# Kernel optimization log

Measured on AMD Instinct MI355X. Metric: run time of the kernel, lower is better.

The kernel has to match this reference:

```python
import jax, jax.numpy as jnp
import numpy as np

N, E, F0, H, D, G, C = 10000, 150000, 128, 8, 64, 64, 10
HD = H * D
SLOPE = 0.01  # LeakyReLU negative slope (alpha)
EPS = 1e-5    # BatchNorm eps


def gat_layer(x, src, dst, W, a_src, a_dst, b):
    # x: [N, Fin] -> out: [N, H*D]; standard multi-head GAT with concat
    n = x.shape[0]
    h = (x @ W).reshape(n, H, D)                       # [N,H,D]
    e_src = jnp.einsum('nhd,hd->nh', h, a_src)         # [N,H]
    e_dst = jnp.einsum('nhd,hd->nh', h, a_dst)
    e = e_src[src] + e_dst[dst]                        # [E,H]
    e = jnp.where(e > 0, e, SLOPE * e)                 # LeakyReLU
    m = jax.ops.segment_max(e, dst, num_segments=n)    # per-dst max for stable softmax
    ex = jnp.exp(e - m[dst])
    denom = jax.ops.segment_sum(ex, dst, num_segments=n)
    att = ex / denom[dst]                              # [E,H]
    msg = h[src] * att[:, :, None]                     # [E,H,D]
    out = jax.ops.segment_sum(msg, dst, num_segments=n).reshape(n, HD)
    return jax.nn.elu(out + b)


def hgnn_forward(x, edge_index, batch,
                 W0, as0, ad0, b0, W1, as1, ad1, b1,
                 W2, as2, ad2, b2, W3, as3, ad3, b3,
                 mW1, mb1, gamma, beta, mW2, mb2):
    src, dst = edge_index[0], edge_index[1]
    x0 = gat_layer(x, src, dst, W0, as0, ad0, b0)      # init_graph
    x1 = gat_layer(x0, src, dst, W1, as1, ad1, b1)     # head
    x2 = gat_layer(x1, src, dst, W2, as2, ad2, b2)     # body
    x3 = x0 + x2                                       # residual
    xt = gat_layer(x3, src, dst, W3, as3, ad3, b3)     # tail
    xc = jnp.concatenate((xt, x1, x2, x3), axis=1)     # [N, 4*HD]
    pooled = jax.ops.segment_max(xc, batch, num_segments=G)
    pooled = jnp.where(jnp.isfinite(pooled), pooled, 0.0)
    # MLP: Linear -> BatchNorm1d (batch-stats) -> ReLU -> Linear
    z = pooled @ mW1 + mb1
    mu = jnp.mean(z, axis=0)
    var = jnp.mean((z - mu) ** 2, axis=0)
    z = (z - mu) / jnp.sqrt(var + EPS) * gamma + beta
    z = jax.nn.relu(z)
    return z @ mW2 + mb2                               # [G, C]


def setup_inputs() -> dict:
    key = jax.random.key(0)
    ks = jax.random.split(key, 12)
    x = jax.random.normal(ks[0], (N, F0), jnp.float32)
    edge_index = jax.random.randint(ks[1], (2, E), 0, N, dtype=jnp.int32)
    batch = jnp.sort(jax.random.randint(ks[2], (N,), 0, G, dtype=jnp.int32))

    def layer_params(k, fin):
        k1, k2, k3 = jax.random.split(k, 3)
        return (0.1 * jax.random.normal(k1, (fin, HD), jnp.float32),
                0.1 * jax.random.normal(k2, (H, D), jnp.float32),
                0.1 * jax.random.normal(k3, (H, D), jnp.float32),
                jnp.zeros((HD,), jnp.float32))

    W0, as0, ad0, b0 = layer_params(ks[3], F0)
    W1, as1, ad1, b1 = layer_params(ks[4], HD)
    W2, as2, ad2, b2 = layer_params(ks[5], HD)
    W3, as3, ad3, b3 = layer_params(ks[6], HD)
    mW1 = 0.05 * jax.random.normal(ks[7], (4 * HD, HD), jnp.float32)
    mb1 = jnp.zeros((HD,), jnp.float32)
    gamma = jnp.ones((HD,), jnp.float32)
    beta = jnp.zeros((HD,), jnp.float32)
    mW2 = 0.05 * jax.random.normal(ks[8], (HD, C), jnp.float32)
    mb2 = jnp.zeros((C,), jnp.float32)
    return dict(x=x, edge_index=edge_index, batch=batch,
                W0=W0, as0=as0, ad0=ad0, b0=b0,
                W1=W1, as1=as1, ad1=ad1, b1=b1,
                W2=W2, as2=as2, ad2=ad2, b2=b2,
                W3=W3, as3=as3, ad3=ad3, b3=b3,
                mW1=mW1, mb1=mb1, gamma=gamma, beta=beta, mW2=mW2, mb2=mb2)


def reference(x, edge_index, batch,
              W0, as0, ad0, b0, W1, as1, ad1, b1,
              W2, as2, ad2, b2, W3, as3, ad3, b3,
              mW1, mb1, gamma, beta, mW2, mb2):
    return hgnn_forward(x, edge_index, batch,
                        W0, as0, ad0, b0, W1, as1, ad1, b1,
                        W2, as2, ad2, b2, W3, as3, ad3, b3,
                        mW1, mb1, gamma, beta, mW2, mb2)
```

## Files before the change

### kernel.cpp

```cpp
#include <hip/hip_runtime.h>

typedef unsigned short u16;
typedef __bf16 bfv8 __attribute__((ext_vector_type(8)));
typedef float f32x16 __attribute__((ext_vector_type(16)));

#define HDIM 512
#define NHEAD 8
#define GNUM 64
#define CNUM 10
#define SLOPE 0.01f
#define BNEPS 1e-5f
#define PSPLIT 8

__device__ __forceinline__ float b2f(u16 u) { return __uint_as_float(((unsigned)u) << 16); }
__device__ __forceinline__ u16 f2b(float f) {
    unsigned u = __float_as_uint(f);
    u += 0x7FFFu + ((u >> 16) & 1u);
    return (u16)(u >> 16);
}
__device__ __forceinline__ void splitbf(float v, u16& hi, u16& lo) {
    u16 h = f2b(v);
    hi = h;
    lo = f2b(v - b2f(h));
}

__global__ void sentinel_kernel(float* out, int n, float val) {
    int i = blockIdx.x * 256 + threadIdx.x;
    if (i < n) out[i] = val;
}

__global__ void zero_i32_kernel(int* __restrict__ p, int n) {
    int i = blockIdx.x * 256 + threadIdx.x;
    if (i < n) p[i] = 0;
}

__device__ __forceinline__ void wsplit_body(const float* __restrict__ W, u16* __restrict__ Whi,
                                            u16* __restrict__ Wlo, int K) {
    __shared__ float tile[64][65];
    int kb = blockIdx.x * 64, nb = blockIdx.y * 64;
    int t = threadIdx.x;
    #pragma unroll
    for (int i = 0; i < 16; i++) {
        int idx = t + i * 256;
        int r = idx >> 6, c = idx & 63;
        tile[r][c] = W[(size_t)(kb + r) * HDIM + nb + c];
    }
    __syncthreads();
    #pragma unroll
    for (int i = 0; i < 16; i++) {
        int idx = t + i * 256;
        int r = idx >> 6, c = idx & 63;
        float v = tile[c][r];
        u16 hi, lo;
        splitbf(v, hi, lo);
        size_t o = (size_t)(nb + r) * K + kb + c;
        Whi[o] = hi;
        Wlo[o] = lo;
    }
}

__global__ void wsplit_kernel(const float* __restrict__ W, u16* __restrict__ Whi,
                              u16* __restrict__ Wlo, int K) {
    wsplit_body(W, Whi, Wlo, K);
}

__global__ void wsplit3_kernel(const float* __restrict__ W1, const float* __restrict__ W2,
                               const float* __restrict__ W3,
                               u16* __restrict__ h1, u16* __restrict__ l1,
                               u16* __restrict__ h2, u16* __restrict__ l2,
                               u16* __restrict__ h3, u16* __restrict__ l3) {
    const float* W = (blockIdx.z == 0) ? W1 : (blockIdx.z == 1) ? W2 : W3;
    u16* Wh = (blockIdx.z == 0) ? h1 : (blockIdx.z == 1) ? h2 : h3;
    u16* Wl = (blockIdx.z == 0) ? l1 : (blockIdx.z == 1) ? l2 : l3;
    wsplit_body(W, Wh, Wl, HDIM);
}

__global__ void xsplit_kernel(const float* __restrict__ x, u16* __restrict__ hi,
                              u16* __restrict__ lo, int n) {
    int i = blockIdx.x * 256 + threadIdx.x;
    if (i < n) splitbf(x[i], hi[i], lo[i]);
}

__global__ __launch_bounds__(256, 3) void gemm_split(const u16* __restrict__ Ah,
                                                     const u16* __restrict__ Al,
                                                     const u16* __restrict__ Bh,
                                                     const u16* __restrict__ Bl,
                                                     const float* __restrict__ a_src,
                                                     const float* __restrict__ a_dst,
                                                     u16* __restrict__ Chi,
                                                     float* __restrict__ es,
                                                     float* __restrict__ ed, int M, int K) {
    __shared__ u16 sAh[128 * 40];
    __shared__ u16 sAl[128 * 40];
    __shared__ u16 sBh[64 * 40];
    __shared__ u16 sBl[64 * 40];
    __shared__ float sE[128][2][2];
    int t = threadIdx.x;
    int id = blockIdx.x;
    int nrt = gridDim.x >> 3;
    int w = (id & 7) * nrt + (id >> 3);
    int rt = w >> 3, ct = w & 7;
    int bm = rt * 128, bn = ct * 64;
    int hh = ct;
    int wv = t >> 6, lane = t & 63;
    int wm = (wv >> 1) * 64, wn = (wv & 1) * 32;
    int l32 = lane & 31, kh = lane >> 5;

    int ar0 = (2 * t) >> 2, ac0 = ((2 * t) & 3) * 8;
    int ar1 = (2 * t + 1) >> 2, ac1 = ((2 * t + 1) & 3) * 8;
    int br = t >> 2, bc = (t & 3) * 8;

    f32x16 acc[2];
    for (int m = 0; m < 2; m++)
        for (int r = 0; r < 16; r++) acc[m][r] = 0.f;

    bool ok0 = (bm + ar0) < M, ok1 = (bm + ar1) < M;
    const u16* Ahp0 = Ah + (size_t)(bm + ar0) * K + ac0;
    const u16* Alp0 = Al + (size_t)(bm + ar0) * K + ac0;
    const u16* Ahp1 = Ah + (size_t)(bm + ar1) * K + ac1;
    const u16* Alp1 = Al + (size_t)(bm + ar1) * K + ac1;
    const u16* Bhp = Bh + (size_t)(bn + br) * K + bc;
    const u16* Blp = Bl + (size_t)(bn + br) * K + bc;

    int4 a0h = make_int4(0, 0, 0, 0), a0l = a0h, a1h = a0h, a1l = a0h;
    if (ok0) { a0h = *(const int4*)(Ahp0); a0l = *(const int4*)(Alp0); }
    if (ok1) { a1h = *(const int4*)(Ahp1); a1l = *(const int4*)(Alp1); }
    int4 bvh = *(const int4*)(Bhp);
    int4 bvl = *(const int4*)(Blp);

    for (int kt = 0; kt < K; kt += 32) {
        __syncthreads();
        *(int4*)&sAh[ar0 * 40 + ac0] = a0h;
        *(int4*)&sAl[ar0 * 40 + ac0] = a0l;
        *(int4*)&sAh[ar1 * 40 + ac1] = a1h;
        *(int4*)&sAl[ar1 * 40 + ac1] = a1l;
        *(int4*)&sBh[br * 40 + bc] = bvh;
        *(int4*)&sBl[br * 40 + bc] = bvl;
        __syncthreads();
        int ktn = kt + 32;
        if (ktn < K) {
            a0h = make_int4(0, 0, 0, 0); a0l = a0h; a1h = a0h; a1l = a0h;
            if (ok0) { a0h = *(const int4*)(Ahp0 + ktn); a0l = *(const int4*)(Alp0 + ktn); }
            if (ok1) { a1h = *(const int4*)(Ahp1 + ktn); a1l = *(const int4*)(Alp1 + ktn); }
            bvh = *(const int4*)(Bhp + ktn);
            bvl = *(const int4*)(Blp + ktn);
        }
        #pragma unroll
        for (int ks = 0; ks < 32; ks += 16) {
            int ko = ks + kh * 8;
            bfv8 a0 = *(bfv8*)&sAh[(wm + l32) * 40 + ko];
            bfv8 a0lo = *(bfv8*)&sAl[(wm + l32) * 40 + ko];
            bfv8 a1 = *(bfv8*)&sAh[(wm + 32 + l32) * 40 + ko];
            bfv8 a1lo = *(bfv8*)&sAl[(wm + 32 + l32) * 40 + ko];
            bfv8 b = *(bfv8*)&sBh[(wn + l32) * 40 + ko];
            bfv8 blo = *(bfv8*)&sBl[(wn + l32) * 40 + ko];
            acc[0] = __builtin_amdgcn_mfma_f32_32x32x16_bf16(a0lo, b, acc[0], 0, 0, 0);
            acc[0] = __builtin_amdgcn_mfma_f32_32x32x16_bf16(a0, blo, acc[0], 0, 0, 0);
            acc[0] = __builtin_amdgcn_mfma_f32_32x32x16_bf16(a0, b, acc[0], 0, 0, 0);
            acc[1] = __builtin_amdgcn_mfma_f32_32x32x16_bf16(a1lo, b, acc[1], 0, 0, 0);
            acc[1] = __builtin_amdgcn_mfma_f32_32x32x16_bf16(a1, blo, acc[1], 0, 0, 0);
            acc[1] = __builtin_amdgcn_mfma_f32_32x32x16_bf16(a1, b, acc[1], 0, 0, 0);
        }
    }
    float asv = a_src[hh * 64 + wn + l32];
    float adv = a_dst[hh * 64 + wn + l32];
    int col = bn + wn + l32;
    #pragma unroll
    for (int mt = 0; mt < 2; mt++)
        #pragma unroll
        for (int r = 0; r < 16; r++) {
            float v = acc[mt][r];
            int lr = wm + mt * 32 + (r & 3) + 8 * (r >> 2) + 4 * kh;
            int row = bm + lr;
            if (row < M) Chi[(size_t)row * HDIM + col] = f2b(v);
            float s1 = v * asv, s2 = v * adv;
            #pragma unroll
            for (int msk = 1; msk <= 16; msk <<= 1) {
                s1 += __shfl_xor(s1, msk);
                s2 += __shfl_xor(s2, msk);
            }
            if (l32 == 0) { sE[lr][wv & 1][0] = s1; sE[lr][wv & 1][1] = s2; }
        }
    __syncthreads();
    if (t < 128) {
        int row = bm + t;
        if (row < M) {
            es[row * NHEAD + hh] = sE[t][0][0] + sE[t][1][0];
            ed[row * NHEAD + hh] = sE[t][0][1] + sE[t][1][1];
        }
    }
}

__global__ void hist_kernel(const int* __restrict__ ei, int* __restrict__ deg, int E) {
    int e = blockIdx.x * 256 + threadIdx.x;
    if (e < E) atomicAdd(&deg[ei[E + e]], 1);
}

__global__ void scan_kernel(const int* __restrict__ deg, int* __restrict__ offs,
                            int* __restrict__ cursor, int n) {
    __shared__ int lds[1024];
    int t = threadIdx.x;
    const int CH = 16;
    int base = t * CH;
    int local[CH];
    int s = 0;
    for (int i = 0; i < CH; i++) {
        int idx = base + i;
        local[i] = (idx < n) ? deg[idx] : 0;
        s += local[i];
    }
    lds[t] = s;
    __syncthreads();
    for (int off = 1; off < 1024; off <<= 1) {
        int v = lds[t];
        int add = (t >= off) ? lds[t - off] : 0;
        __syncthreads();
        lds[t] = v + add;
        __syncthreads();
    }
    int ex = (t == 0) ? 0 : lds[t - 1];
    for (int i = 0; i < CH; i++) {
        int idx = base + i;
        if (idx < n) { offs[idx] = ex; cursor[idx] = ex; ex += local[i]; }
    }
}

__global__ void scatter_kernel(const int* __restrict__ ei, int* __restrict__ cursor,
                               int* __restrict__ ssrc, int E) {
    int e = blockIdx.x * 256 + threadIdx.x;
    if (e < E) {
        int p = atomicAdd(&cursor[ei[E + e]], 1);
        ssrc[p] = ei[e];
    }
}

__global__ void agg_kernel(const u16* __restrict__ hh_buf, const float* __restrict__ es,
                           const float* __restrict__ ed, const int* __restrict__ offs,
                           const int* __restrict__ deg, const int* __restrict__ ssrc,
                           const float* __restrict__ bias,
                           u16* __restrict__ ohi, u16* __restrict__ olo,
                           const u16* __restrict__ rhi, const u16* __restrict__ rlo,
                           u16* __restrict__ qhi, u16* __restrict__ qlo, int n) {
    int node = blockIdx.x * 4 + (threadIdx.x >> 6);
    int lane = threadIdx.x & 63;
    if (node >= n) return;
    int hh = lane >> 3, f = lane * 8;
    float edv = ed[node * NHEAD + hh];
    int st = offs[node], cnt = deg[node];

    float m = -INFINITY, den = 0.f;
    float acc[8] = {0.f, 0.f, 0.f, 0.f, 0.f, 0.f, 0.f, 0.f};
    int i = 0;
    for (; i + 2 <= cnt; i += 2) {
        int s0 = ssrc[st + i];
        int s1 = ssrc[st + i + 1];
        float e0 = es[s0 * NHEAD + hh] + edv;
        float e1 = es[s1 * NHEAD + hh] + edv;
        union { int4 v; u16 u[8]; } U0, U1;
        U0.v = *(const int4*)(hh_buf + (size_t)s0 * HDIM + f);
        U1.v = *(const int4*)(hh_buf + (size_t)s1 * HDIM + f);
        e0 = e0 > 0.f ? e0 : SLOPE * e0;
        e1 = e1 > 0.f ? e1 : SLOPE * e1;
        float mn = fmaxf(m, fmaxf(e0, e1));
        float sc = __expf(m - mn);
        float w0 = __expf(e0 - mn);
        float w1 = __expf(e1 - mn);
        den = den * sc + w0 + w1;
        #pragma unroll
        for (int j = 0; j < 8; j++)
            acc[j] = acc[j] * sc + w0 * b2f(U0.u[j]) + w1 * b2f(U1.u[j]);
        m = mn;
    }
    if (i < cnt) {
        int s0 = ssrc[st + i];
        float e0 = es[s0 * NHEAD + hh] + edv;
        union { int4 v; u16 u[8]; } U0;
        U0.v = *(const int4*)(hh_buf + (size_t)s0 * HDIM + f);
        e0 = e0 > 0.f ? e0 : SLOPE * e0;
        float mn = fmaxf(m, e0);
        float sc = __expf(m - mn);
        float w0 = __expf(e0 - mn);
        den = den * sc + w0;
        #pragma unroll
        for (int j = 0; j < 8; j++) acc[j] = acc[j] * sc + w0 * b2f(U0.u[j]);
    }
    float inv = den > 0.f ? 1.f / den : 0.f;
    union { int4 v; u16 u[8]; } Hi, Lo;
    float o[8];
    #pragma unroll
    for (int j = 0; j < 8; j++) {
        float v = acc[j] * inv + bias[f + j];
        o[j] = v > 0.f ? v : __expf(v) - 1.f;
        splitbf(o[j], Hi.u[j], Lo.u[j]);
    }
    size_t base = (size_t)node * HDIM + f;
    *(int4*)&ohi[base] = Hi.v;
    *(int4*)&olo[base] = Lo.v;
    if (rhi) {
        union { int4 v; u16 u[8]; } Rh, Rl, Qh, Ql;
        Rh.v = *(const int4*)&rhi[base];
        Rl.v = *(const int4*)&rlo[base];
        #pragma unroll
        for (int j = 0; j < 8; j++) {
            float v = o[j] + b2f(Rh.u[j]) + b2f(Rl.u[j]);
            splitbf(v, Qh.u[j], Ql.u[j]);
        }
        *(int4*)&qhi[base] = Qh.v;
        *(int4*)&qlo[base] = Ql.v;
    }
}

__global__ void pool1_kernel(const u16* __restrict__ s0h, const u16* __restrict__ s1h,
                             const u16* __restrict__ s2h, const u16* __restrict__ s3h,
                             const int* __restrict__ batch, float* __restrict__ partial, int n) {
    int g = blockIdx.x, b = blockIdx.y, c = blockIdx.z;
    int t = threadIdx.x;
    const u16* hs[4] = {s0h, s1h, s2h, s3h};
    const u16* sh = hs[b];
    int lo = 0, hi = n;
    while (lo < hi) { int mid = (lo + hi) >> 1; if (batch[mid] < g) lo = mid + 1; else hi = mid; }
    int start = lo;
    lo = start; hi = n;
    while (lo < hi) { int mid = (lo + hi) >> 1; if (batch[mid] < g + 1) lo = mid + 1; else hi = mid; }
    int end = lo;
    int len = end - start;
    int cb = start + (int)(((long long)len * c) / PSPLIT);
    int ce = start + (int)(((long long)len * (c + 1)) / PSPLIT);
    float mx0 = -INFINITY, mx1 = -INFINITY;
    for (int i = cb; i < ce; i++) {
        size_t ro = (size_t)i * HDIM;
        mx0 = fmaxf(mx0, b2f(sh[ro + t]));
        mx1 = fmaxf(mx1, b2f(sh[ro + 256 + t]));
    }
    size_t pb = (size_t)((g * 4 + b) * PSPLIT + c) * 512;
    partial[pb + t] = mx0;
    partial[pb + 256 + t] = mx1;
}

__global__ void pool2_kernel(const float* __restrict__ partial, float* __restrict__ pooled,
                             const float* __restrict__ mb1, float* __restrict__ z) {
    int g = blockIdx.x, b = blockIdx.y;
    int t = threadIdx.x;
    float mx0 = -INFINITY, mx1 = -INFINITY;
    for (int c = 0; c < PSPLIT; c++) {
        size_t pb = (size_t)((g * 4 + b) * PSPLIT + c) * 512;
        mx0 = fmaxf(mx0, partial[pb + t]);
        mx1 = fmaxf(mx1, partial[pb + 256 + t]);
    }
    if (!isfinite(mx0)) mx0 = 0.f;
    if (!isfinite(mx1)) mx1 = 0.f;
    pooled[g * 2048 + b * 512 + t] = mx0;
    pooled[g * 2048 + b * 512 + 256 + t] = mx1;
    if (t < 128) {
        int col = b * 128 + t;
        z[g * HDIM + col] = mb1[col];
    }
}

__global__ __launch_bounds__(256) void mlp1_splitk(const float* __restrict__ pooled,
                                                   const float* __restrict__ mW1,
                                                   float* __restrict__ z) {
    __shared__ float sp[256];
    int g = blockIdx.x, kc = blockIdx.y * 256;
    int t = threadIdx.x;
    sp[t] = pooled[g * 2048 + kc + t];
    __syncthreads();
    float acc0 = 0.f, acc1 = 0.f;
    const float* wp = mW1 + (size_t)kc * HDIM;
    #pragma unroll 8
    for (int k = 0; k < 256; k++) {
        float pv = sp[k];
        acc0 += pv * wp[(size_t)k * HDIM + t];
        acc1 += pv * wp[(size_t)k * HDIM + 256 + t];
    }
    atomicAdd(&z[g * HDIM + t], acc0);
    atomicAdd(&z[g * HDIM + 256 + t], acc1);
}

__global__ void bn_relu_kernel(const float* __restrict__ z, const float* __restrict__ gammaf,
                               const float* __restrict__ betaf, float* __restrict__ zn) {
    int col = blockIdx.x;
    int g = threadIdx.x;
    float v = z[g * HDIM + col];
    float s = v;
    for (int o = 32; o > 0; o >>= 1) s += __shfl_xor(s, o);
    float mu = s * (1.f / 64.f);
    float d = v - mu;
    float s2 = d * d;
    for (int o = 32; o > 0; o >>= 1) s2 += __shfl_xor(s2, o);
    float var = s2 * (1.f / 64.f);
    float o = d * rsqrtf(var + BNEPS) * gammaf[col] + betaf[col];
    zn[g * HDIM + col] = fmaxf(o, 0.f);
}

__global__ void final_kernel(const float* __restrict__ zn, const float* __restrict__ mW2,
                             const float* __restrict__ mb2, float* __restrict__ out) {
    int g = blockIdx.x, c = blockIdx.y;
    int lane = threadIdx.x;
    float acc = 0.f;
    #pragma unroll
    for (int k = lane; k < HDIM; k += 64) acc += zn[g * HDIM + k] * mW2[k * CNUM + c];
    for (int o = 32; o > 0; o >>= 1) acc += __shfl_down(acc, o);
    if (lane == 0) out[g * CNUM + c] = acc + mb2[c];
}

extern "C" void kernel_launch(void* const* d_in, const int* in_sizes, int n_in,
                              void* d_out, int out_size, void* d_ws, size_t ws_size,
                              hipStream_t stream) {
    const float* x = (const float*)d_in[0];
    const int* ei = (const int*)d_in[1];
    const int* batch = (const int*)d_in[2];
    const float* Wm[4] = {(const float*)d_in[3], (const float*)d_in[7],
                          (const float*)d_in[11], (const float*)d_in[15]};
    const float* Asc[4] = {(const float*)d_in[4], (const float*)d_in[8],
                           (const float*)d_in[12], (const float*)d_in[16]};
    const float* Adc[4] = {(const float*)d_in[5], (const float*)d_in[9],
                           (const float*)d_in[13], (const float*)d_in[17]};
    const float* Bb[4] = {(const float*)d_in[6], (const float*)d_in[10],
                          (const float*)d_in[14], (const float*)d_in[18]};
    const float* mW1 = (const float*)d_in[19];
    const float* mb1 = (const float*)d_in[20];
    const float* gammaf = (const float*)d_in[21];
    const float* betaf = (const float*)d_in[22];
    const float* mW2 = (const float*)d_in[23];
    const float* mb2 = (const float*)d_in[24];
    (void)n_in;

    int N = in_sizes[2];
    int E = in_sizes[1] / 2;
    int F0 = in_sizes[0] / N;

    char* p = (char*)d_ws;
    auto alloc = [&](size_t bytes) -> char* {
        char* r = p;
        p += (bytes + 255) & ~(size_t)255;
        return r;
    };
    u16 *Wh[4], *Wl[4];
    Wh[0] = (u16*)alloc((size_t)HDIM * F0 * 2);
    Wl[0] = (u16*)alloc((size_t)HDIM * F0 * 2);
    for (int l = 1; l < 4; l++) {
        Wh[l] = (u16*)alloc((size_t)HDIM * HDIM * 2);
        Wl[l] = (u16*)alloc((size_t)HDIM * HDIM * 2);
    }
    u16* xinh = (u16*)alloc((size_t)N * F0 * 2);
    u16* xinl = (u16*)alloc((size_t)N * F0 * 2);
    u16* hhi = (u16*)alloc((size_t)N * HDIM * 2);
    u16 *xh[4], *xl[4];
    for (int l = 0; l < 4; l++) {
        xh[l] = (u16*)alloc((size_t)N * HDIM * 2);
        xl[l] = (u16*)alloc((size_t)N * HDIM * 2);
    }
    float* es = (float*)alloc((size_t)N * NHEAD * 4);
    float* ed = (float*)alloc((size_t)N * NHEAD * 4);
    int* deg = (int*)alloc((size_t)N * 4);
    int* offs = (int*)alloc((size_t)N * 4);
    int* cursor = (int*)alloc((size_t)N * 4);
    int* ssrc = (int*)alloc((size_t)E * 4);
    float* partial = (float*)alloc((size_t)GNUM * 4 * PSPLIT * 512 * 4);
    float* pooled = (float*)alloc((size_t)GNUM * 4 * HDIM * 4);
    float* z = (float*)alloc((size_t)GNUM * HDIM * 4);
    float* zn = (float*)alloc((size_t)GNUM * HDIM * 4);

    if ((size_t)(p - (char*)d_ws) > ws_size) {
        sentinel_kernel<<<(out_size + 255) / 256, 256, 0, stream>>>((float*)d_out, out_size, 999.f);
        return;
    }

    {
        dim3 wg0(F0 / 64, HDIM / 64);
        wsplit_kernel<<<wg0, 256, 0, stream>>>(Wm[0], Wh[0], Wl[0], F0);
        dim3 wg3(HDIM / 64, HDIM / 64, 3);
        wsplit3_kernel<<<wg3, 256, 0, stream>>>(Wm[1], Wm[2], Wm[3],
                                                Wh[1], Wl[1], Wh[2], Wl[2], Wh[3], Wl[3]);
    }
    xsplit_kernel<<<(N * F0 + 255) / 256, 256, 0, stream>>>(x, xinh, xinl, N * F0);

    zero_i32_kernel<<<(N + 255) / 256, 256, 0, stream>>>(deg, N);
    hist_kernel<<<(E + 255) / 256, 256, 0, stream>>>(ei, deg, E);
    scan_kernel<<<1, 1024, 0, stream>>>(deg, offs, cursor, N);
    scatter_kernel<<<(E + 255) / 256, 256, 0, stream>>>(ei, cursor, ssrc, E);

    const u16* linh[4] = {xinh, xh[0], xh[1], xh[3]};
    const u16* linl[4] = {xinl, xl[0], xl[1], xl[3]};
    int lK[4] = {F0, HDIM, HDIM, HDIM};
    u16* louth[4] = {xh[0], xh[1], xh[2], xh[0]};
    u16* loutl[4] = {xl[0], xl[1], xl[2], xl[0]};
    int nrt = (N + 127) / 128;
    int gemm_blocks = nrt * 8;
    int agg_blocks = (N + 3) / 4;
    for (int L = 0; L < 4; L++) {
        gemm_split<<<gemm_blocks, 256, 0, stream>>>(linh[L], linl[L], Wh[L], Wl[L],
                                                    Asc[L], Adc[L], hhi, es, ed, N, lK[L]);
        const u16* rh = (L == 2) ? xh[0] : nullptr;
        const u16* rl = (L == 2) ? xl[0] : nullptr;
        u16* qh = (L == 2) ? xh[3] : nullptr;
        u16* ql = (L == 2) ? xl[3] : nullptr;
        agg_kernel<<<agg_blocks, 256, 0, stream>>>(hhi, es, ed, offs, deg, ssrc, Bb[L],
                                                   louth[L], loutl[L], rh, rl, qh, ql, N);
    }

    dim3 pool1_grid(GNUM, 4, PSPLIT);
    pool1_kernel<<<pool1_grid, 256, 0, stream>>>(xh[0], xh[1], xh[2], xh[3],
                                                 batch, partial, N);
    dim3 pool2_grid(GNUM, 4);
    pool2_kernel<<<pool2_grid, 256, 0, stream>>>(partial, pooled, mb1, z);

    dim3 mlp_grid(GNUM, 8);
    mlp1_splitk<<<mlp_grid, 256, 0, stream>>>(pooled, mW1, z);
    bn_relu_kernel<<<HDIM, 64, 0, stream>>>(z, gammaf, betaf, zn);
    dim3 final_grid(GNUM, CNUM);
    final_kernel<<<final_grid, 64, 0, stream>>>(zn, mW2, mb2, (float*)d_out);
}
```

Measured before the change: 436.3 us.

## Load GEMM MFMA operands directly from global memory, dropping LDS staging

The split-bf16 GEMM no longer stages A and B tiles through shared memory with double-buffered register prefetch and two barriers per k-step. Each lane now loads its MFMA fragments straight from global memory, and the hi/lo MFMAs for the two row tiles are interleaved. Activation buffers are padded to a multiple of 128 rows and the tail is zeroed, so the unguarded loads stay in bounds. Operands that were shared through LDS are now fetched redundantly by several waves from global or cache, and launch bounds drop occupancy from 3 to 2 blocks.

```diff
diff --git a/kernel.cpp b/kernel.cpp
--- a/kernel.cpp
+++ b/kernel.cpp
@@ -32,6 +32,24 @@
 __global__ void zero_i32_kernel(int* __restrict__ p, int n) {
     int i = blockIdx.x * 256 + threadIdx.x;
     if (i < n) p[i] = 0;
+}
+
+__global__ void ztail_kernel(u16* __restrict__ xinh, u16* __restrict__ xinl, int F0,
+                             u16* __restrict__ x0h, u16* __restrict__ x0l,
+                             u16* __restrict__ x1h, u16* __restrict__ x1l,
+                             u16* __restrict__ x2h, u16* __restrict__ x2l,
+                             u16* __restrict__ x3h, u16* __restrict__ x3l, int N) {
+    int row = N + blockIdx.x;
+    int b = blockIdx.y;
+    int t = threadIdx.x;
+    if (b < 2) {
+        u16* p = (b == 0) ? xinh : xinl;
+        for (int c = t; c < F0; c += 256) p[(size_t)row * F0 + c] = 0;
+    } else {
+        u16* ps[8] = {x0h, x0l, x1h, x1l, x2h, x2l, x3h, x3l};
+        u16* p = ps[b - 2];
+        for (int c = t; c < HDIM; c += 256) p[(size_t)row * HDIM + c] = 0;
+    }
 }
 
 __device__ __forceinline__ void wsplit_body(const float* __restrict__ W, u16* __restrict__ Whi,
@@ -81,7 +99,7 @@
     if (i < n) splitbf(x[i], hi[i], lo[i]);
 }
 
-__global__ __launch_bounds__(256, 3) void gemm_split(const u16* __restrict__ Ah,
+__global__ __launch_bounds__(256, 2) void gemm_split(const u16* __restrict__ Ah,
                                                      const u16* __restrict__ Al,
                                                      const u16* __restrict__ Bh,
                                                      const u16* __restrict__ Bl,
@@ -90,10 +108,6 @@
                                                      u16* __restrict__ Chi,
                                                      float* __restrict__ es,
                                                      float* __restrict__ ed, int M, int K) {
-    __shared__ u16 sAh[128 * 40];
-    __shared__ u16 sAl[128 * 40];
-    __shared__ u16 sBh[64 * 40];
-    __shared__ u16 sBl[64 * 40];
     __shared__ float sE[128][2][2];
     int t = threadIdx.x;
     int id = blockIdx.x;
@@ -106,61 +120,43 @@
     int wm = (wv >> 1) * 64, wn = (wv & 1) * 32;
     int l32 = lane & 31, kh = lane >> 5;
 
-    int ar0 = (2 * t) >> 2, ac0 = ((2 * t) & 3) * 8;
-    int ar1 = (2 * t + 1) >> 2, ac1 = ((2 * t + 1) & 3) * 8;
-    int br = t >> 2, bc = (t & 3) * 8;
-
     f32x16 acc[2];
     for (int m = 0; m < 2; m++)
         for (int r = 0; r < 16; r++) acc[m][r] = 0.f;
 
-    bool ok0 = (bm + ar0) < M, ok1 = (bm + ar1) < M;
-    const u16* Ahp0 = Ah + (size_t)(bm + ar0) * K + ac0;
-    const u16* Alp0 = Al + (size_t)(bm + ar0) * K + ac0;
-    const u16* Ahp1 = Ah + (size_t)(bm + ar1) * K + ac1;
-    const u16* Alp1 = Al + (size_t)(bm + ar1) * K + ac1;
-    const u16* Bhp = Bh + (size_t)(bn + br) * K + bc;
-    const u16* Blp = Bl + (size_t)(bn + br) * K + bc;
-
-    int4 a0h = make_int4(0, 0, 0, 0), a0l = a0h, a1h = a0h, a1l = a0h;
-    if (ok0) { a0h = *(const int4*)(Ahp0); a0l = *(const int4*)(Alp0); }
-    if (ok1) { a1h = *(const int4*)(Ahp1); a1l = *(const int4*)(Alp1); }
-    int4 bvh = *(const int4*)(Bhp);
-    int4 bvl = *(const int4*)(Blp);
-
+    const u16* pAh0 = Ah + (size_t)(bm + wm + l32) * K + kh * 8;
+    const u16* pAl0 = Al + (size_t)(bm + wm + l32) * K + kh * 8;
+    const u16* pAh1 = pAh0 + (size_t)32 * K;
+    const u16* pAl1 = pAl0 + (size_t)32 * K;
+    const u16* pBh = Bh + (size_t)(bn + wn + l32) * K + kh * 8;
+    const u16* pBl = Bl + (size_t)(bn + wn + l32) * K + kh * 8;
+
+    #pragma unroll 2
     for (int kt = 0; kt < K; kt += 32) {
-        __syncthreads();
-        *(int4*)&sAh[ar0 * 40 + ac0] = a0h;
-        *(int4*)&sAl[ar0 * 40 + ac0] = a0l;
-        *(int4*)&sAh[ar1 * 40 + ac1] = a1h;
-        *(int4*)&sAl[ar1 * 40 + ac1] = a1l;
-        *(int4*)&sBh[br * 40 + bc] = bvh;
-        *(int4*)&sBl[br * 40 + bc] = bvl;
-        __syncthreads();
-        int ktn = kt + 32;
-        if (ktn < K) {
-            a0h = make_int4(0, 0, 0, 0); a0l = a0h; a1h = a0h; a1l = a0h;
-            if (ok0) { a0h = *(const int4*)(Ahp0 + ktn); a0l = *(const int4*)(Alp0 + ktn); }
-            if (ok1) { a1h = *(const int4*)(Ahp1 + ktn); a1l = *(const int4*)(Alp1 + ktn); }
-            bvh = *(const int4*)(Bhp + ktn);
-            bvl = *(const int4*)(Blp + ktn);
-        }
-        #pragma unroll
-        for (int ks = 0; ks < 32; ks += 16) {
-            int ko = ks + kh * 8;
-            bfv8 a0 = *(bfv8*)&sAh[(wm + l32) * 40 + ko];
-            bfv8 a0lo = *(bfv8*)&sAl[(wm + l32) * 40 + ko];
-            bfv8 a1 = *(bfv8*)&sAh[(wm + 32 + l32) * 40 + ko];
-            bfv8 a1lo = *(bfv8*)&sAl[(wm + 32 + l32) * 40 + ko];
-            bfv8 b = *(bfv8*)&sBh[(wn + l32) * 40 + ko];
-            bfv8 blo = *(bfv8*)&sBl[(wn + l32) * 40 + ko];
-            acc[0] = __builtin_amdgcn_mfma_f32_32x32x16_bf16(a0lo, b, acc[0], 0, 0, 0);
-            acc[0] = __builtin_amdgcn_mfma_f32_32x32x16_bf16(a0, blo, acc[0], 0, 0, 0);
-            acc[0] = __builtin_amdgcn_mfma_f32_32x32x16_bf16(a0, b, acc[0], 0, 0, 0);
-            acc[1] = __builtin_amdgcn_mfma_f32_32x32x16_bf16(a1lo, b, acc[1], 0, 0, 0);
-            acc[1] = __builtin_amdgcn_mfma_f32_32x32x16_bf16(a1, blo, acc[1], 0, 0, 0);
-            acc[1] = __builtin_amdgcn_mfma_f32_32x32x16_bf16(a1, b, acc[1], 0, 0, 0);
-        }
+        bfv8 a0h0 = *(const bfv8*)(pAh0 + kt);
+        bfv8 a0l0 = *(const bfv8*)(pAl0 + kt);
+        bfv8 a1h0 = *(const bfv8*)(pAh1 + kt);
+        bfv8 a1l0 = *(const bfv8*)(pAl1 + kt);
+        bfv8 bh0  = *(const bfv8*)(pBh + kt);
+        bfv8 bl0  = *(const bfv8*)(pBl + kt);
+        bfv8 a0h1 = *(const bfv8*)(pAh0 + kt + 16);
+        bfv8 a0l1 = *(const bfv8*)(pAl0 + kt + 16);
+        bfv8 a1h1 = *(const bfv8*)(pAh1 + kt + 16);
+        bfv8 a1l1 = *(const bfv8*)(pAl1 + kt + 16);
+        bfv8 bh1  = *(const bfv8*)(pBh + kt + 16);
+        bfv8 bl1  = *(const bfv8*)(pBl + kt + 16);
+        acc[0] = __builtin_amdgcn_mfma_f32_32x32x16_bf16(a0l0, bh0, acc[0], 0, 0, 0);
+        acc[1] = __builtin_amdgcn_mfma_f32_32x32x16_bf16(a1l0, bh0, acc[1], 0, 0, 0);
+        acc[0] = __builtin_amdgcn_mfma_f32_32x32x16_bf16(a0h0, bl0, acc[0], 0, 0, 0);
+        acc[1] = __builtin_amdgcn_mfma_f32_32x32x16_bf16(a1h0, bl0, acc[1], 0, 0, 0);
+        acc[0] = __builtin_amdgcn_mfma_f32_32x32x16_bf16(a0h0, bh0, acc[0], 0, 0, 0);
+        acc[1] = __builtin_amdgcn_mfma_f32_32x32x16_bf16(a1h0, bh0, acc[1], 0, 0, 0);
+        acc[0] = __builtin_amdgcn_mfma_f32_32x32x16_bf16(a0l1, bh1, acc[0], 0, 0, 0);
+        acc[1] = __builtin_amdgcn_mfma_f32_32x32x16_bf16(a1l1, bh1, acc[1], 0, 0, 0);
+        acc[0] = __builtin_amdgcn_mfma_f32_32x32x16_bf16(a0h1, bl1, acc[0], 0, 0, 0);
+        acc[1] = __builtin_amdgcn_mfma_f32_32x32x16_bf16(a1h1, bl1, acc[1], 0, 0, 0);
+        acc[0] = __builtin_amdgcn_mfma_f32_32x32x16_bf16(a0h1, bh1, acc[0], 0, 0, 0);
+        acc[1] = __builtin_amdgcn_mfma_f32_32x32x16_bf16(a1h1, bh1, acc[1], 0, 0, 0);
     }
     float asv = a_src[hh * 64 + wn + l32];
     float adv = a_dst[hh * 64 + wn + l32];
@@ -429,6 +425,8 @@
     int N = in_sizes[2];
     int E = in_sizes[1] / 2;
     int F0 = in_sizes[0] / N;
+    int nrt = (N + 127) / 128;
+    int N128 = nrt * 128;
 
     char* p = (char*)d_ws;
     auto alloc = [&](size_t bytes) -> char* {
@@ -443,13 +441,13 @@
         Wh[l] = (u16*)alloc((size_t)HDIM * HDIM * 2);
         Wl[l] = (u16*)alloc((size_t)HDIM * HDIM * 2);
     }
-    u16* xinh = (u16*)alloc((size_t)N * F0 * 2);
-    u16* xinl = (u16*)alloc((size_t)N * F0 * 2);
+    u16* xinh = (u16*)alloc((size_t)N128 * F0 * 2);
+    u16* xinl = (u16*)alloc((size_t)N128 * F0 * 2);
     u16* hhi = (u16*)alloc((size_t)N * HDIM * 2);
     u16 *xh[4], *xl[4];
     for (int l = 0; l < 4; l++) {
-        xh[l] = (u16*)alloc((size_t)N * HDIM * 2);
-        xl[l] = (u16*)alloc((size_t)N * HDIM * 2);
+        xh[l] = (u16*)alloc((size_t)N128 * HDIM * 2);
+        xl[l] = (u16*)alloc((size_t)N128 * HDIM * 2);
     }
     float* es = (float*)alloc((size_t)N * NHEAD * 4);
     float* ed = (float*)alloc((size_t)N * NHEAD * 4);
@@ -475,6 +473,11 @@
                                                 Wh[1], Wl[1], Wh[2], Wl[2], Wh[3], Wl[3]);
     }
     xsplit_kernel<<<(N * F0 + 255) / 256, 256, 0, stream>>>(x, xinh, xinl, N * F0);
+    if (N128 > N) {
+        dim3 zt(N128 - N, 10);
+        ztail_kernel<<<zt, 256, 0, stream>>>(xinh, xinl, F0, xh[0], xl[0], xh[1], xl[1],
+                                             xh[2], xl[2], xh[3], xl[3], N);
+    }
 
     zero_i32_kernel<<<(N + 255) / 256, 256, 0, stream>>>(deg, N);
     hist_kernel<<<(E + 255) / 256, 256, 0, stream>>>(ei, deg, E);
@@ -486,7 +489,6 @@
     int lK[4] = {F0, HDIM, HDIM, HDIM};
     u16* louth[4] = {xh[0], xh[1], xh[2], xh[0]};
     u16* loutl[4] = {xl[0], xl[1], xl[2], xl[0]};
-    int nrt = (N + 127) / 128;
     int gemm_blocks = nrt * 8;
     int agg_blocks = (N + 3) / 4;
     for (int L = 0; L < 4; L++) {
```

New measurement: 562.8 us. +29.0%, slower.
